# Performance work log

Measured on AMD Instinct MI355X. Metric: run time of the kernel, lower is better.

## Reference

```python
import jax, jax.numpy as jnp
import numpy as np

B, S, D, H = 4, 2048, 1024, 16
HD = D // H  # head_dim = 64


def setup_inputs() -> dict:
    key = jax.random.key(0)
    ks = jax.random.split(key, 5)
    scale = 0.02
    return {
        "x": jax.random.normal(ks[0], (B, S, D), dtype=jnp.float32),
        "Wq": jax.random.normal(ks[1], (D, D), dtype=jnp.float32) * scale,
        "Wk": jax.random.normal(ks[2], (D, D), dtype=jnp.float32) * scale,
        "Wv": jax.random.normal(ks[3], (D, D), dtype=jnp.float32) * scale,
        "Wo": jax.random.normal(ks[4], (D, D), dtype=jnp.float32) * scale,
        "bo": jnp.zeros((D,), dtype=jnp.float32),
    }


def reference(x, Wq, Wk, Wv, Wo, bo):
    b, s, d = x.shape
    # projections (no bias on q/k/v, matching qkv_bias=False)
    q = (x @ Wq).reshape(b, s, H, HD).transpose(0, 2, 1, 3)  # [B,H,S,HD]
    k = (x @ Wk).reshape(b, s, H, HD).transpose(0, 2, 1, 3)
    v = (x @ Wv).reshape(b, s, H, HD).transpose(0, 2, 1, 3)
    scores = jnp.einsum("bhqd,bhkd->bhqk", q, k) / jnp.sqrt(jnp.float32(HD))
    causal = jnp.tril(jnp.ones((s, s), dtype=bool))  # True = keep
    scores = jnp.where(causal, scores, -jnp.inf)
    attn = jax.nn.softmax(scores, axis=-1)
    # dropout p=0.0 -> identity
    out = jnp.einsum("bhqk,bhkd->bhqd", attn, v)
    out = out.transpose(0, 2, 1, 3).reshape(b, s, d)
    return out @ Wo + bo
```

## Files before the change

### kernel.cpp

```cpp
#include <hip/hip_runtime.h>

typedef unsigned short u16;
typedef unsigned int u32;
typedef __attribute__((ext_vector_type(4))) float f32x4;
typedef __attribute__((ext_vector_type(16))) float f32x16;
typedef __attribute__((ext_vector_type(8))) __bf16 bf16x8;
typedef __attribute__((ext_vector_type(4))) _Float16 f16x4;
typedef __attribute__((ext_vector_type(8))) _Float16 f16x8;
typedef __attribute__((ext_vector_type(4))) u16 u16x4;
typedef __attribute__((ext_vector_type(4))) u32 u32x4;
typedef __attribute__((ext_vector_type(2))) u32 u32x2;

#define D_ 1024
#define S_ 2048
#define B_ 4
#define H_ 16
#define HD_ 64
#define M_ 8192
#define LDP 72
#define QSCALE 0.18033688011112042591f

__device__ __forceinline__ u16 f2bf(float f) {
  u32 u = __float_as_uint(f);
  u += 0x7fffu + ((u >> 16) & 1u);
  return (u16)(u >> 16);
}

__device__ __forceinline__ float max3f(float a, float b, float c) {
  return fmaxf(fmaxf(a, b), c);
}

__device__ __forceinline__ void gload_lds16(const void* g, void* l) {
  __builtin_amdgcn_global_load_lds((const __attribute__((address_space(1))) void*)g,
                                   (__attribute__((address_space(3))) void*)l, 16, 0, 0);
}

__global__ __launch_bounds__(256) void prep_kernel(const float* __restrict__ x, u16* __restrict__ xb,
                                                   const float* __restrict__ Wq, const float* __restrict__ Wk,
                                                   const float* __restrict__ Wv, const float* __restrict__ Wo,
                                                   u16* __restrict__ Wqt, u16* __restrict__ Wkt,
                                                   u16* __restrict__ Wvt, u16* __restrict__ Wot) {
  __shared__ float lds[64][65];
  int lin = blockIdx.x;
  if (lin < 8192) {
    int i = (lin * 256 + threadIdx.x) * 4;
    f32x4 v = *(const f32x4*)(x + i);
    u16x4 o = {f2bf(v[0]), f2bf(v[1]), f2bf(v[2]), f2bf(v[3])};
    *(u16x4*)(xb + i) = o;
    return;
  }
  int pos = lin - 8192;
  int z = pos >> 8, rem = pos & 255;
  const float* W = z == 0 ? Wq : z == 1 ? Wk : z == 2 ? Wv : Wo;
  u16* Wt       = z == 0 ? Wqt : z == 1 ? Wkt : z == 2 ? Wvt : Wot;
  int k0 = (rem >> 4) * 64, n0 = (rem & 15) * 64;
  int tr = threadIdx.x >> 6, tc = threadIdx.x & 63;
#pragma unroll
  for (int i = 0; i < 16; ++i)
    lds[tr + i * 4][tc] = W[(size_t)(k0 + tr + i * 4) * D_ + n0 + tc];
  __syncthreads();
#pragma unroll
  for (int i = 0; i < 16; ++i)
    Wt[(size_t)(n0 + tr + i * 4) * D_ + k0 + tc] = f2bf(lds[tc][tr + i * 4]);
}

__device__ __forceinline__ void gemm_main(const u16* __restrict__ A, const u16* __restrict__ Bt,
                                          u16* As, u16* Bs, int row0, int col0, f32x4 acc[4][4]) {
  const int tid = threadIdx.x;
  const int lane = tid & 63, wave = tid >> 6;
  const int wr = wave >> 1, wc = wave & 1;
  const int l15 = lane & 15, lg = lane >> 4;
  const int sr8 = lane >> 3;
  const int scx = (lane & 7) ^ sr8;
#pragma unroll 1
  for (int k0 = 0; k0 < D_; k0 += 64) {
#pragma unroll
    for (int it = 0; it < 4; ++it) {
      int rbase = (it * 4 + wave) * 8;
      int r = rbase + sr8;
      gload_lds16(A + (size_t)(row0 + r) * D_ + k0 + scx * 8, As + rbase * 64);
      gload_lds16(Bt + (size_t)(col0 + r) * D_ + k0 + scx * 8, Bs + rbase * 64);
    }
    __syncthreads();
#pragma unroll
    for (int kk = 0; kk < 64; kk += 32) {
      const int cb = kk >> 3;
      bf16x8 af[4], bf[4];
#pragma unroll
      for (int m = 0; m < 4; ++m) {
        int row = wr * 64 + m * 16 + l15;
        af[m] = *(const bf16x8*)(As + row * 64 + (((cb + lg) ^ (l15 & 7)) << 3));
      }
#pragma unroll
      for (int n = 0; n < 4; ++n) {
        int row = wc * 64 + n * 16 + l15;
        bf[n] = *(const bf16x8*)(Bs + row * 64 + (((cb + lg) ^ (l15 & 7)) << 3));
      }
#pragma unroll
      for (int m = 0; m < 4; ++m)
#pragma unroll
        for (int n = 0; n < 4; ++n)
          acc[m][n] = __builtin_amdgcn_mfma_f32_16x16x32_bf16(af[m], bf[n], acc[m][n], 0, 0, 0);
    }
    __syncthreads();
  }
}

__global__ __launch_bounds__(256) void qkv_gemm_kernel(const u16* __restrict__ xb,
                                                       const u16* __restrict__ Wqt, const u16* __restrict__ Wkt,
                                                       const u16* __restrict__ Wvt,
                                                       u16* __restrict__ Qb, u16* __restrict__ Kb,
                                                       _Float16* __restrict__ Vt) {
  __shared__ u16 As[128 * 64];
  __shared__ u16 Bs[128 * 64];
  int lin = blockIdx.x;
  int xcd = lin & 7, pos = lin >> 3;
  int mode = pos / 64;
  int rem = pos & 63;
  int by = xcd * 8 + (rem >> 3);
  int bx = rem & 7;
  const u16* Bt = mode == 0 ? Wqt : mode == 1 ? Wkt : Wvt;
  f32x4 acc[4][4] = {};
  int row0 = by * 128, col0 = bx * 128;
  gemm_main(xb, Bt, As, Bs, row0, col0, acc);
  int lane = threadIdx.x & 63, wave = threadIdx.x >> 6;
  int wr = wave >> 1, wc = wave & 1, l15 = lane & 15, lg = lane >> 4;
  int rbase = row0 + wr * 64 + lg * 4, cbase = col0 + wc * 64 + l15;
  if (mode == 2) {
#pragma unroll
    for (int m = 0; m < 4; ++m) {
      int row = rbase + m * 16;
      int b = row >> 11, s = row & (S_ - 1);
#pragma unroll
      for (int n = 0; n < 4; ++n) {
        int col = cbase + n * 16;
        int h = col >> 6, hd = col & 63;
        f16x4 vv = {(_Float16)acc[m][n][0], (_Float16)acc[m][n][1],
                    (_Float16)acc[m][n][2], (_Float16)acc[m][n][3]};
        *(f16x4*)(Vt + ((size_t)((b << 4) + h) * HD_ + hd) * S_ + s) = vv;
      }
    }
  } else {
    u16* dst = mode == 0 ? Qb : Kb;
    float scl = mode == 0 ? QSCALE : 1.0f;
#pragma unroll
    for (int m = 0; m < 4; ++m)
#pragma unroll
      for (int n = 0; n < 4; ++n) {
        int col = cbase + n * 16;
#pragma unroll
        for (int r = 0; r < 4; ++r) {
          int row = rbase + m * 16 + r;
          dst[(size_t)row * D_ + col] = f2bf(acc[m][n][r] * scl);
        }
      }
  }
}

__global__ __launch_bounds__(128) void attn_kernel(const u16* __restrict__ Qb, const u16* __restrict__ Kb,
                                                   const _Float16* __restrict__ Vt, u16* __restrict__ attnb) {
  __shared__ u16 Ks[64][LDP];
  __shared__ _Float16 Vs[64][LDP];
  const int tid = threadIdx.x;
  const int wave = tid >> 6, lane = tid & 63;
  const int l31 = lane & 31, hi = lane >> 5;
  const int lin = blockIdx.x;
  const int xcd = lin & 7, slot = lin >> 3;
  const int qblk = 31 - (slot >> 3);
  const int bh = (slot & 7) * 8 + xcd;
  const int b = bh >> 4, h = bh & 15;
  const int ntiles = qblk + 1;
  const int wq0 = qblk * 64 + wave * 32;
  const int qg = wq0 + l31;

  const int srow = tid >> 1;
  const int sh = (tid & 1) * 32;
  const u16* Kp = Kb + (size_t)(b * S_ + srow) * D_ + h * HD_ + sh;
  const _Float16* Vp = Vt + ((size_t)bh * HD_ + srow) * S_ + sh;

  const u16* Qrow = Qb + (size_t)(b * S_ + qg) * D_ + h * HD_;
  bf16x8 qf[4];
#pragma unroll
  for (int ds = 0; ds < 4; ++ds)
    qf[ds] = *(const bf16x8*)(Qrow + ds * 16 + hi * 8);

  float m = -1e30f, lsum = 0.f;
  f32x16 oL = {}, oH = {};
  u32x4 kst[4], vst[4];

#pragma unroll
  for (int c = 0; c < 4; ++c) {
    kst[c] = *(const u32x4*)(Kp + c * 8);
    vst[c] = *(const u32x4*)(Vp + c * 8);
  }
  Kp += (size_t)64 * D_;
  Vp += 64;

#pragma unroll 1
  for (int t = 0; t < ntiles; ++t) {
    __syncthreads();
#pragma unroll
    for (int c = 0; c < 4; ++c) {
      *(u32x4*)(&Ks[srow][sh + c * 8]) = kst[c];
      *(u32x4*)(&Vs[srow][sh + c * 8]) = vst[c];
    }
    __syncthreads();
    if (t + 1 < ntiles) {
#pragma unroll
      for (int c = 0; c < 4; ++c) {
        kst[c] = *(const u32x4*)(Kp + c * 8);
        vst[c] = *(const u32x4*)(Vp + c * 8);
      }
      Kp += (size_t)64 * D_;
      Vp += 64;
    }
    f32x16 sA = {}, sB = {};
    __builtin_amdgcn_s_setprio(1);
#pragma unroll
    for (int ds = 0; ds < 4; ++ds) {
      bf16x8 k0 = *(const bf16x8*)(&Ks[l31][ds * 16 + hi * 8]);
      bf16x8 k1 = *(const bf16x8*)(&Ks[32 + l31][ds * 16 + hi * 8]);
      sA = __builtin_amdgcn_mfma_f32_32x32x16_bf16(k0, qf[ds], sA, 0, 0, 0);
      sB = __builtin_amdgcn_mfma_f32_32x32x16_bf16(k1, qf[ds], sB, 0, 0, 0);
    }
    __builtin_amdgcn_s_setprio(0);
    if (t == ntiles - 1) {
      const int kvb = t * 64;
#pragma unroll
      for (int r = 0; r < 16; ++r) {
        int off = (r & 3) + 8 * (r >> 2) + 4 * hi;
        if (kvb + off > qg) sA[r] = -1e30f;
        if (kvb + 32 + off > qg) sB[r] = -1e30f;
      }
    }
    float mx[16];
#pragma unroll
    for (int r = 0; r < 16; ++r) mx[r] = fmaxf(sA[r], sB[r]);
    float y0 = max3f(mx[0], mx[1], mx[2]);
    float y1 = max3f(mx[3], mx[4], mx[5]);
    float y2 = max3f(mx[6], mx[7], mx[8]);
    float y3 = max3f(mx[9], mx[10], mx[11]);
    float y4 = max3f(mx[12], mx[13], mx[14]);
    float tmax = fmaxf(max3f(y0, y1, y2), max3f(y3, y4, mx[15]));
    tmax = fmaxf(tmax, __shfl_xor(tmax, 32));
    if (!__all(tmax - m <= 8.f)) {
      float nm = fmaxf(m, tmax);
      float alpha = exp2f(m - nm);
      m = nm;
      lsum *= alpha;
      oL *= alpha;
      oH *= alpha;
    }
    float psum = 0.f;
#pragma unroll
    for (int r = 0; r < 16; ++r) {
      sA[r] = exp2f(sA[r] - m);
      sB[r] = exp2f(sB[r] - m);
      psum += sA[r] + sB[r];
    }
    lsum += psum;
    u32 uA[8], uB[8], vA[8], vB[8];
#pragma unroll
    for (int k = 0; k < 8; ++k) {
      uA[k] = __builtin_bit_cast(u32, __builtin_amdgcn_cvt_pkrtz(sA[2 * k], sA[2 * k + 1]));
      uB[k] = __builtin_bit_cast(u32, __builtin_amdgcn_cvt_pkrtz(sB[2 * k], sB[2 * k + 1]));
    }
#pragma unroll
    for (int k = 0; k < 8; ++k) {
      vA[k] = __shfl_xor(uA[k], 32);
      vB[k] = __shfl_xor(uB[k], 32);
    }
    __builtin_amdgcn_s_setprio(1);
#pragma unroll
    for (int ks = 0; ks < 4; ++ks) {
      const u32* U = (ks >> 1) ? uB : uA;
      const u32* Vw = (ks >> 1) ? vB : vA;
      const int b4 = (ks & 1) * 4;
      u32 w0 = hi ? Vw[b4 + 2] : U[b4 + 0];
      u32 w1 = hi ? Vw[b4 + 3] : U[b4 + 1];
      u32 w2 = hi ? U[b4 + 2] : Vw[b4 + 0];
      u32 w3 = hi ? U[b4 + 3] : Vw[b4 + 1];
      f16x8 pa = __builtin_bit_cast(f16x8, (u32x4){w0, w1, w2, w3});
      f16x8 v0 = *(const f16x8*)(&Vs[l31][ks * 16 + hi * 8]);
      f16x8 v1 = *(const f16x8*)(&Vs[32 + l31][ks * 16 + hi * 8]);
      oL = __builtin_amdgcn_mfma_f32_32x32x16_f16(v0, pa, oL, 0, 0, 0);
      oH = __builtin_amdgcn_mfma_f32_32x32x16_f16(v1, pa, oH, 0, 0, 0);
    }
    __builtin_amdgcn_s_setprio(0);
  }

  lsum += __shfl_xor(lsum, 32);
  float inv = 1.0f / lsum;
  __syncthreads();
  u16* scr = &Ks[wave * 32 + l31][0];
#pragma unroll
  for (int a = 0; a < 4; ++a) {
    u16x4 pl = {f2bf(oL[4 * a + 0] * inv), f2bf(oL[4 * a + 1] * inv),
                f2bf(oL[4 * a + 2] * inv), f2bf(oL[4 * a + 3] * inv)};
    *(u16x4*)(scr + 8 * a + 4 * hi) = pl;
    u16x4 ph = {f2bf(oH[4 * a + 0] * inv), f2bf(oH[4 * a + 1] * inv),
                f2bf(oH[4 * a + 2] * inv), f2bf(oH[4 * a + 3] * inv)};
    *(u16x4*)(scr + 32 + 8 * a + 4 * hi) = ph;
  }
  asm volatile("s_waitcnt lgkmcnt(0)" ::: "memory");
  const u16* srd = &Ks[wave * 32 + l31][hi * 32];
  u16* Og = attnb + (size_t)(b * S_ + wq0 + l31) * D_ + h * HD_ + hi * 32;
#pragma unroll
  for (int c = 0; c < 4; ++c)
    *(u32x4*)(Og + c * 8) = *(const u32x4*)(srd + c * 8);
}

__global__ __launch_bounds__(256) void out_gemm_kernel(const u16* __restrict__ attnb, const u16* __restrict__ Wot,
                                                       const float* __restrict__ bo, float* __restrict__ outp) {
  __shared__ u16 As[128 * 64];
  __shared__ u16 Bs[128 * 64];
  int lin = blockIdx.x;
  int xcd = lin & 7, pos = lin >> 3;
  int by = xcd * 8 + (pos >> 3);
  int bx = pos & 7;
  f32x4 acc[4][4] = {};
  int row0 = by * 128, col0 = bx * 128;
  gemm_main(attnb, Wot, As, Bs, row0, col0, acc);
  int lane = threadIdx.x & 63, wave = threadIdx.x >> 6;
  int wr = wave >> 1, wc = wave & 1, l15 = lane & 15, lg = lane >> 4;
  int rbase = row0 + wr * 64 + lg * 4, cbase = col0 + wc * 64 + l15;
#pragma unroll
  for (int n = 0; n < 4; ++n) {
    float bn = bo[cbase + n * 16];
#pragma unroll
    for (int m = 0; m < 4; ++m)
#pragma unroll
      for (int r = 0; r < 4; ++r)
        outp[(size_t)(rbase + m * 16 + r) * D_ + cbase + n * 16] = acc[m][n][r] + bn;
  }
}

extern "C" void kernel_launch(void* const* d_in, const int* in_sizes, int n_in,
                              void* d_out, int out_size, void* d_ws, size_t ws_size,
                              hipStream_t stream) {
  const float* x  = (const float*)d_in[0];
  const float* Wq = (const float*)d_in[1];
  const float* Wk = (const float*)d_in[2];
  const float* Wv = (const float*)d_in[3];
  const float* Wo = (const float*)d_in[4];
  const float* bo = (const float*)d_in[5];
  float* outp = (float*)d_out;

  char* ws = (char*)d_ws;
  u16* xb        = (u16*)(ws);
  u16* Wqt       = (u16*)(ws + ((size_t)16 << 20));
  u16* Wkt       = (u16*)(ws + ((size_t)18 << 20));
  u16* Wvt       = (u16*)(ws + ((size_t)20 << 20));
  u16* Wot       = (u16*)(ws + ((size_t)22 << 20));
  u16* Qb        = (u16*)(ws + ((size_t)24 << 20));
  u16* Kb        = (u16*)(ws + ((size_t)40 << 20));
  _Float16* Vt   = (_Float16*)(ws + ((size_t)56 << 20));
  u16* attnb     = (u16*)(ws + ((size_t)72 << 20));

  prep_kernel<<<dim3(9216), dim3(256), 0, stream>>>(x, xb, Wq, Wk, Wv, Wo, Wqt, Wkt, Wvt, Wot);
  qkv_gemm_kernel<<<dim3(1536), dim3(256), 0, stream>>>(xb, Wqt, Wkt, Wvt, Qb, Kb, Vt);
  attn_kernel<<<dim3(2048), dim3(128), 0, stream>>>(Qb, Kb, Vt, attnb);
  out_gemm_kernel<<<dim3(512), dim3(256), 0, stream>>>(attnb, Wot, bo, outp);
}
```

Before: 187.7 us.

## Compute softmax row sums via MFMA with ones and peel masked last tile

Replaces the scalar per-tile exp-sum accumulation and final cross-half shuffle with an extra MFMA that multiplies the fp16 probability fragment by a ones matrix, so every lane gets the row sum. The last causal tile is peeled out of the loop so the steady-state loop carries no mask check or prefetch branch. This trades VALU adds for one more MFMA per k-step, about 50% more PV matrix work, and the sum now comes from fp16-rounded probabilities.

```diff
diff --git a/kernel.cpp b/kernel.cpp
--- a/kernel.cpp
+++ b/kernel.cpp
@@ -184,36 +184,14 @@
   for (int ds = 0; ds < 4; ++ds)
     qf[ds] = *(const bf16x8*)(Qrow + ds * 16 + hi * 8);
 
-  float m = -1e30f, lsum = 0.f;
+  float m = -1e30f;
   f32x16 oL = {}, oH = {};
+  f32x16 osum = {};
+  const f16x8 ones8 = {(_Float16)1.f, (_Float16)1.f, (_Float16)1.f, (_Float16)1.f,
+                       (_Float16)1.f, (_Float16)1.f, (_Float16)1.f, (_Float16)1.f};
   u32x4 kst[4], vst[4];
 
-#pragma unroll
-  for (int c = 0; c < 4; ++c) {
-    kst[c] = *(const u32x4*)(Kp + c * 8);
-    vst[c] = *(const u32x4*)(Vp + c * 8);
-  }
-  Kp += (size_t)64 * D_;
-  Vp += 64;
-
-#pragma unroll 1
-  for (int t = 0; t < ntiles; ++t) {
-    __syncthreads();
-#pragma unroll
-    for (int c = 0; c < 4; ++c) {
-      *(u32x4*)(&Ks[srow][sh + c * 8]) = kst[c];
-      *(u32x4*)(&Vs[srow][sh + c * 8]) = vst[c];
-    }
-    __syncthreads();
-    if (t + 1 < ntiles) {
-#pragma unroll
-      for (int c = 0; c < 4; ++c) {
-        kst[c] = *(const u32x4*)(Kp + c * 8);
-        vst[c] = *(const u32x4*)(Vp + c * 8);
-      }
-      Kp += (size_t)64 * D_;
-      Vp += 64;
-    }
+  auto tile_body = [&](int kvb, bool domask) {
     f32x16 sA = {}, sB = {};
     __builtin_amdgcn_s_setprio(1);
 #pragma unroll
@@ -224,8 +202,7 @@
       sB = __builtin_amdgcn_mfma_f32_32x32x16_bf16(k1, qf[ds], sB, 0, 0, 0);
     }
     __builtin_amdgcn_s_setprio(0);
-    if (t == ntiles - 1) {
-      const int kvb = t * 64;
+    if (domask) {
 #pragma unroll
       for (int r = 0; r < 16; ++r) {
         int off = (r & 3) + 8 * (r >> 2) + 4 * hi;
@@ -247,18 +224,15 @@
       float nm = fmaxf(m, tmax);
       float alpha = exp2f(m - nm);
       m = nm;
-      lsum *= alpha;
+      osum *= alpha;
       oL *= alpha;
       oH *= alpha;
     }
-    float psum = 0.f;
 #pragma unroll
     for (int r = 0; r < 16; ++r) {
       sA[r] = exp2f(sA[r] - m);
       sB[r] = exp2f(sB[r] - m);
-      psum += sA[r] + sB[r];
-    }
-    lsum += psum;
+    }
     u32 uA[8], uB[8], vA[8], vB[8];
 #pragma unroll
     for (int k = 0; k < 8; ++k) {
@@ -285,12 +259,48 @@
       f16x8 v1 = *(const f16x8*)(&Vs[32 + l31][ks * 16 + hi * 8]);
       oL = __builtin_amdgcn_mfma_f32_32x32x16_f16(v0, pa, oL, 0, 0, 0);
       oH = __builtin_amdgcn_mfma_f32_32x32x16_f16(v1, pa, oH, 0, 0, 0);
+      osum = __builtin_amdgcn_mfma_f32_32x32x16_f16(ones8, pa, osum, 0, 0, 0);
     }
     __builtin_amdgcn_s_setprio(0);
-  }
-
-  lsum += __shfl_xor(lsum, 32);
-  float inv = 1.0f / lsum;
+  };
+
+#pragma unroll
+  for (int c = 0; c < 4; ++c) {
+    kst[c] = *(const u32x4*)(Kp + c * 8);
+    vst[c] = *(const u32x4*)(Vp + c * 8);
+  }
+  Kp += (size_t)64 * D_;
+  Vp += 64;
+
+#pragma unroll 1
+  for (int t = 0; t < ntiles - 1; ++t) {
+    __syncthreads();
+#pragma unroll
+    for (int c = 0; c < 4; ++c) {
+      *(u32x4*)(&Ks[srow][sh + c * 8]) = kst[c];
+      *(u32x4*)(&Vs[srow][sh + c * 8]) = vst[c];
+    }
+    __syncthreads();
+#pragma unroll
+    for (int c = 0; c < 4; ++c) {
+      kst[c] = *(const u32x4*)(Kp + c * 8);
+      vst[c] = *(const u32x4*)(Vp + c * 8);
+    }
+    Kp += (size_t)64 * D_;
+    Vp += 64;
+    tile_body(t * 64, false);
+  }
+
+  __syncthreads();
+#pragma unroll
+  for (int c = 0; c < 4; ++c) {
+    *(u32x4*)(&Ks[srow][sh + c * 8]) = kst[c];
+    *(u32x4*)(&Vs[srow][sh + c * 8]) = vst[c];
+  }
+  __syncthreads();
+  tile_body((ntiles - 1) * 64, true);
+
+  float inv = 1.0f / osum[0];
   __syncthreads();
   u16* scr = &Ks[wave * 32 + l31][0];
 #pragma unroll
```

Result: no change. 184.7 us, median of 2 (-1.6%).
